# Performance work log

Hardware: AMD Instinct MI355X
Metric: run time of the kernel (lower is better)

Reference implementation:

```python
import jax, jax.numpy as jnp
import numpy as np

DIM = 384
HEADS = 12
HEAD_DIM = DIM // HEADS
WS = 7


def setup_inputs() -> dict:
    key = jax.random.key(0)
    k0, k1, k2, k3, k4 = jax.random.split(key, 5)
    x = jax.random.normal(k0, (16, DIM, 56, 56), dtype=jnp.float32)
    s = 1.0 / np.sqrt(DIM)
    Wqkv = jax.random.normal(k1, (DIM, 3 * DIM), dtype=jnp.float32) * s
    bqkv = jax.random.normal(k2, (3 * DIM,), dtype=jnp.float32) * 0.01
    Wproj = jax.random.normal(k3, (DIM, DIM), dtype=jnp.float32) * s
    bproj = jax.random.normal(k4, (DIM,), dtype=jnp.float32) * 0.01
    return {"x": x, "Wqkv": Wqkv, "bqkv": bqkv, "Wproj": Wproj, "bproj": bproj}


def _window_attention(x, Wqkv, bqkv, Wproj, bproj):
    B, D, H, W = x.shape
    x = jnp.transpose(x, (0, 2, 3, 1))  # (B, H, W, D)
    pad_h = (WS - H % WS) % WS
    pad_w = (WS - W % WS) % WS
    if pad_h or pad_w:
        x = jnp.pad(x, ((0, 0), (0, pad_h), (0, pad_w), (0, 0)))
    Hp, Wp = x.shape[1], x.shape[2]
    nH, nW = Hp // WS, Wp // WS
    # window partition: (B*nH*nW, WS*WS, D)
    xw = x.reshape(B, nH, WS, nW, WS, D).transpose(0, 1, 3, 2, 4, 5)
    windows = xw.reshape(B * nH * nW, WS * WS, D)
    BnW, N, _ = windows.shape
    qkv = windows @ Wqkv + bqkv  # (BnW, N, 3D)
    qkv = qkv.reshape(BnW, N, 3, HEADS, HEAD_DIM).transpose(2, 0, 3, 1, 4)
    q, k, v = qkv[0], qkv[1], qkv[2]  # (BnW, heads, N, hd)
    scale = HEAD_DIM ** -0.5
    attn = jnp.einsum('bhnd,bhmd->bhnm', q, k) * scale
    attn = jax.nn.softmax(attn, axis=-1)
    out = jnp.einsum('bhnm,bhmd->bhnd', attn, v)  # (BnW, heads, N, hd)
    out = out.transpose(0, 2, 1, 3).reshape(BnW, N, D)
    out = out @ Wproj + bproj
    # window reverse
    x = out.reshape(B, nH, nW, WS, WS, D).transpose(0, 1, 3, 2, 4, 5)
    x = x.reshape(B, Hp, Wp, D)
    if pad_h or pad_w:
        x = x[:, :H, :W, :]
    return jnp.transpose(x, (0, 3, 1, 2))  # (B, D, H, W)


def reference(x, Wqkv, bqkv, Wproj, bproj):
    return _window_attention(x, Wqkv, bqkv, Wproj, bproj)
```

## Files before the change

### kernel.cpp

```cpp
#include <hip/hip_runtime.h>

#define TOK     50176
#define NQKV    1152
#define DMODEL  384
#define HW      3136
#define NWIN    1024

typedef __bf16 bf16x8 __attribute__((ext_vector_type(8)));
typedef float  f32x4  __attribute__((ext_vector_type(4)));

__device__ __forceinline__ __bf16 f2bf(float f) {
  unsigned u = __float_as_uint(f);
  u += 0x7fffu + ((u >> 16) & 1u);
  unsigned short s = (unsigned short)(u >> 16);
  return __builtin_bit_cast(__bf16, s);
}
__device__ __forceinline__ unsigned short f2bfu(float f) {
  return __builtin_bit_cast(unsigned short, f2bf(f));
}
__device__ __forceinline__ float bf2f(__bf16 b) {
  return __uint_as_float(((unsigned)__builtin_bit_cast(unsigned short, b)) << 16);
}
__device__ __forceinline__ void gload_lds16(const void* g, void* l) {
  __builtin_amdgcn_global_load_lds(
      (const __attribute__((address_space(1))) unsigned int*)g,
      (__attribute__((address_space(3))) unsigned int*)l, 16, 0, 0);
}

__global__ __launch_bounds__(256) void gather_x(const float* __restrict__ x,
                                                __bf16* __restrict__ Xw) {
  __shared__ __bf16 lt[392 * 48];
  const int ct = blockIdx.x, hr = blockIdx.y, b = blockIdx.z;
  const int tid = threadIdx.x;
  const float* xb = x + ((size_t)(b * 384 + ct * 48)) * HW + hr * 7 * 56;

  for (int u = tid; u < 48 * 7 * 14; u += 256) {
    const int ch = u / 98, rem = u % 98;
    const int h7 = rem / 14, w4 = rem % 14;
    const float4 v = *(const float4*)&xb[(size_t)ch * HW + h7 * 56 + 4 * w4];
    const float vv[4] = {v.x, v.y, v.z, v.w};
#pragma unroll
    for (int e = 0; e < 4; ++e) {
      const int w = 4 * w4 + e;
      const int t = (w / 7) * 49 + h7 * 7 + (w % 7);
      lt[t * 48 + ch] = f2bf(vv[e]);
    }
  }
  __syncthreads();

  const size_t tokbase = (size_t)(b * 64 + hr * 8) * 49;
  for (int u = tid; u < 392 * 6; u += 256) {
    const int t = u / 6, c6 = u % 6;
    const bf16x8 vv = *(const bf16x8*)&lt[t * 48 + 8 * c6];
    *(bf16x8*)&Xw[(tokbase + t) * DMODEL + ct * 48 + 8 * c6] = vv;
  }
}

__global__ __launch_bounds__(256) void unscatter(const __bf16* __restrict__ P,
                                                 float* __restrict__ out) {
  __shared__ __bf16 lt[392 * 48];
  const int ct = blockIdx.x, hr = blockIdx.y, b = blockIdx.z;
  const int tid = threadIdx.x;
  const size_t tokbase = (size_t)(b * 64 + hr * 8) * 49;

  for (int u = tid; u < 392 * 6; u += 256) {
    const int t = u / 6, c6 = u % 6;
    *(bf16x8*)&lt[t * 48 + 8 * c6] =
        *(const bf16x8*)&P[(tokbase + t) * DMODEL + ct * 48 + 8 * c6];
  }
  __syncthreads();

  float* ob = out + ((size_t)(b * 384 + ct * 48)) * HW + hr * 7 * 56;
  for (int u = tid; u < 48 * 98; u += 256) {
    const int ch = u / 98, rem = u % 98;
    const int h7 = rem / 14, w4 = rem % 14;
    float4 o;
    float* oo = (float*)&o;
#pragma unroll
    for (int e = 0; e < 4; ++e) {
      const int w = 4 * w4 + e;
      const int t = (w / 7) * 49 + h7 * 7 + (w % 7);
      oo[e] = bf2f(lt[t * 48 + ch]);
    }
    *(float4*)&ob[(size_t)ch * HW + h7 * 56 + 4 * w4] = o;
  }
}

__global__ void conv_w(const float* __restrict__ Wqkv, const float* __restrict__ Wproj,
                       __bf16* __restrict__ WqkvT, __bf16* __restrict__ WprojT) {
  const int idx = blockIdx.x * 256 + threadIdx.x;
  if (idx < DMODEL * NQKV) {
    const int k = idx / NQKV, n = idx % NQKV;
    WqkvT[(size_t)n * DMODEL + k] = f2bf(Wqkv[idx]);
  }
  if (idx < DMODEL * DMODEL) {
    const int k = idx / DMODEL, n = idx % DMODEL;
    WprojT[(size_t)n * DMODEL + k] = f2bf(Wproj[idx]);
  }
}

__global__ __launch_bounds__(512) void gemm256(const __bf16* __restrict__ A,
                                               const __bf16* __restrict__ BT,
                                               const float* __restrict__ bias,
                                               __bf16* __restrict__ Cout, int Ncols) {
  __shared__ __align__(16) __bf16 As[2][256 * 32];
  __shared__ __align__(16) __bf16 Bs[2][128 * 32];
  const int tid  = threadIdx.x;
  const int lane = tid & 63;
  const int wid  = tid >> 6;

  const int nwg  = gridDim.x * gridDim.y;
  const int orig = blockIdx.y * gridDim.x + blockIdx.x;
  const int q    = nwg >> 3, r = nwg & 7;
  const int xcd  = orig & 7, pos = orig >> 3;
  const int start = (xcd < r) ? xcd * (q + 1) : r * (q + 1) + (xcd - r) * q;
  const int w    = start + pos;
  const int bn   = (w % gridDim.x) << 7;
  const int bm   = (w / gridDim.x) << 8;

  const __bf16* a0 = A  + (size_t)(bm +       (tid >> 2)) * DMODEL + ((tid & 3) << 3);
  const __bf16* a1 = A  + (size_t)(bm + 128 + (tid >> 2)) * DMODEL + ((tid & 3) << 3);
  const __bf16* b0 = BT + (size_t)(bn +       (tid >> 2)) * DMODEL + ((tid & 3) << 3);

  const int wm = (wid >> 1) << 6;
  const int wn = (wid & 1) << 6;
  const int lrow = lane & 15;
  const int lk8  = (lane >> 4) << 3;

  f32x4 acc[4][4] = {};

  auto stage = [&](int buf, int kt) {
    const int koff = kt << 5;
    gload_lds16(a0 + koff, &As[buf][(wid << 9)]);
    gload_lds16(a1 + koff, &As[buf][4096 + (wid << 9)]);
    gload_lds16(b0 + koff, &Bs[buf][(wid << 9)]);
  };

  stage(0, 0);
#pragma unroll 1
  for (int kt = 0; kt < 12; ++kt) {
    __syncthreads();
    if (kt + 1 < 12) stage((kt + 1) & 1, kt + 1);
    const __bf16* pA = &As[kt & 1][(wm + lrow) * 32 + lk8];
    const __bf16* pB = &Bs[kt & 1][(wn + lrow) * 32 + lk8];
    bf16x8 av[4], bv[4];
#pragma unroll
    for (int i = 0; i < 4; ++i) av[i] = *(const bf16x8*)(pA + i * 16 * 32);
#pragma unroll
    for (int j = 0; j < 4; ++j) bv[j] = *(const bf16x8*)(pB + j * 16 * 32);
#pragma unroll
    for (int i = 0; i < 4; ++i)
#pragma unroll
      for (int j = 0; j < 4; ++j)
        acc[j][i] = __builtin_amdgcn_mfma_f32_16x16x32_bf16(bv[j], av[i], acc[j][i], 0, 0, 0);
  }

  const int lr = lane & 15, g = lane >> 4;
  const int tok0 = bm + wm + lr;
  const int ch0  = bn + wn + (g << 2);

#pragma unroll
  for (int j = 0; j < 4; ++j) {
    const int ch = ch0 + 16 * j;
    const float4 b4 = *(const float4*)&bias[ch];
#pragma unroll
    for (int i = 0; i < 4; ++i) {
      const int token = tok0 + 16 * i;
      ushort4 pk;
      pk.x = f2bfu(acc[j][i][0] + b4.x);
      pk.y = f2bfu(acc[j][i][1] + b4.y);
      pk.z = f2bfu(acc[j][i][2] + b4.z);
      pk.w = f2bfu(acc[j][i][3] + b4.w);
      *(ushort4*)&Cout[(size_t)token * Ncols + ch] = pk;
    }
  }
}

__global__ __launch_bounds__(64) void attn_mfma(const __bf16* __restrict__ qkv,
                                                __bf16* __restrict__ attnO) {
  __shared__ __align__(16) __bf16 lds[96 * 72];
  __bf16* p_lds = lds;
  __bf16* vt    = lds + 64 * 72;

  const int lane = threadIdx.x;
  const int win  = blockIdx.x;
  const int h    = blockIdx.y;
  const int lr = lane & 15, g = lane >> 4;
  const size_t rowbase = (size_t)win * 49;

  int rr[4];
#pragma unroll
  for (int f = 0; f < 4; ++f) rr[f] = (16 * f + lr > 48) ? 48 : (16 * f + lr);

  const int co = h * 32 + 8 * g;

  bf16x8 av[4], bv[4];
#pragma unroll
  for (int f = 0; f < 4; ++f) {
    const __bf16* rp = qkv + (rowbase + rr[f]) * NQKV + co;
    av[f] = *(const bf16x8*)(rp + 384);
    bv[f] = *(const bf16x8*)(rp);
  }

  ushort4 vreg[7];
#pragma unroll
  for (int u = 0; u < 7; ++u) {
    const int unit = lane + (u << 6);
    if (unit < 392) {
      const int k = unit >> 3, dq = unit & 7;
      vreg[u] = *(const ushort4*)(qkv + (rowbase + k) * NQKV + 768 + h * 32 + 4 * dq);
    }
  }

  f32x4 acc[4][4] = {};
#pragma unroll
  for (int i = 0; i < 4; ++i)
#pragma unroll
    for (int j = 0; j < 4; ++j)
      acc[i][j] = __builtin_amdgcn_mfma_f32_16x16x32_bf16(av[i], bv[j], acc[i][j], 0, 0, 0);

  const float scale = 0.17677669529663687f;
#pragma unroll
  for (int i = 0; i < 4; ++i)
#pragma unroll
    for (int j = 0; j < 4; ++j)
#pragma unroll
      for (int r = 0; r < 4; ++r) {
        float v = acc[i][j][r] * scale;
        if (i == 3 && (4 * g + r) != 0) v = -1e30f;
        acc[i][j][r] = v;
      }

#pragma unroll
  for (int u = 0; u < 7; ++u) {
    const int unit = lane + (u << 6);
    if (unit < 392) {
      const int k = unit >> 3, dq = unit & 7;
      const ushort4 vv = vreg[u];
      vt[(4 * dq + 0) * 72 + k] = __builtin_bit_cast(__bf16, vv.x);
      vt[(4 * dq + 1) * 72 + k] = __builtin_bit_cast(__bf16, vv.y);
      vt[(4 * dq + 2) * 72 + k] = __builtin_bit_cast(__bf16, vv.z);
      vt[(4 * dq + 3) * 72 + k] = __builtin_bit_cast(__bf16, vv.w);
    }
  }

#pragma unroll
  for (int j = 0; j < 4; ++j) {
    float mx = -1e30f;
#pragma unroll
    for (int i = 0; i < 4; ++i)
#pragma unroll
      for (int r = 0; r < 4; ++r) mx = fmaxf(mx, acc[i][j][r]);
    mx = fmaxf(mx, __shfl_xor(mx, 16));
    mx = fmaxf(mx, __shfl_xor(mx, 32));
    float sum = 0.f;
#pragma unroll
    for (int i = 0; i < 4; ++i)
#pragma unroll
      for (int r = 0; r < 4; ++r) {
        const float e = __expf(acc[i][j][r] - mx);
        acc[i][j][r] = e;
        sum += e;
      }
    sum += __shfl_xor(sum, 16);
    sum += __shfl_xor(sum, 32);
    const float inv = 1.f / sum;
#pragma unroll
    for (int i = 0; i < 4; ++i) {
      ushort4 pk;
      pk.x = f2bfu(acc[i][j][0] * inv);
      pk.y = f2bfu(acc[i][j][1] * inv);
      pk.z = f2bfu(acc[i][j][2] * inv);
      pk.w = f2bfu(acc[i][j][3] * inv);
      *(ushort4*)&p_lds[(16 * j + lr) * 72 + 16 * i + 4 * g] = pk;
    }
  }

  f32x4 o[2][4] = {};
#pragma unroll
  for (int ks = 0; ks < 2; ++ks) {
    bf16x8 a2[2], b2[4];
#pragma unroll
    for (int i2 = 0; i2 < 2; ++i2)
      a2[i2] = *(const bf16x8*)&vt[(16 * i2 + lr) * 72 + 32 * ks + 8 * g];
#pragma unroll
    for (int j2 = 0; j2 < 4; ++j2)
      b2[j2] = *(const bf16x8*)&p_lds[(16 * j2 + lr) * 72 + 32 * ks + 8 * g];
#pragma unroll
    for (int i2 = 0; i2 < 2; ++i2)
#pragma unroll
      for (int j2 = 0; j2 < 4; ++j2)
        o[i2][j2] = __builtin_amdgcn_mfma_f32_16x16x32_bf16(a2[i2], b2[j2], o[i2][j2], 0, 0, 0);
  }

#pragma unroll
  for (int j2 = 0; j2 < 4; ++j2) {
    const int q = 16 * j2 + lr;
    if (q <= 48) {
#pragma unroll
      for (int i2 = 0; i2 < 2; ++i2) {
        ushort4 ok;
        ok.x = f2bfu(o[i2][j2][0]);
        ok.y = f2bfu(o[i2][j2][1]);
        ok.z = f2bfu(o[i2][j2][2]);
        ok.w = f2bfu(o[i2][j2][3]);
        *(ushort4*)&attnO[(rowbase + q) * DMODEL + h * 32 + 16 * i2 + 4 * g] = ok;
      }
    }
  }
}

extern "C" void kernel_launch(void* const* d_in, const int* in_sizes, int n_in,
                              void* d_out, int out_size, void* d_ws, size_t ws_size,
                              hipStream_t stream) {
  const float* x     = (const float*)d_in[0];
  const float* Wqkv  = (const float*)d_in[1];
  const float* bqkv  = (const float*)d_in[2];
  const float* Wproj = (const float*)d_in[3];
  const float* bproj = (const float*)d_in[4];
  float* out = (float*)d_out;

  char* ws = (char*)d_ws;
  __bf16* Xw     = (__bf16*)ws;  ws += (size_t)TOK * DMODEL * 2;
  __bf16* qkvb   = (__bf16*)ws;  ws += (size_t)TOK * NQKV * 2;
  __bf16* attnO  = (__bf16*)ws;  ws += (size_t)TOK * DMODEL * 2;
  __bf16* attnP  = (__bf16*)ws;  ws += (size_t)TOK * DMODEL * 2;
  __bf16* WqkvT  = (__bf16*)ws;  ws += (size_t)NQKV * DMODEL * 2;
  __bf16* WprojT = (__bf16*)ws;

  gather_x<<<dim3(8, 8, 16), 256, 0, stream>>>(x, Xw);
  conv_w<<<1728, 256, 0, stream>>>(Wqkv, Wproj, WqkvT, WprojT);
  gemm256<<<dim3(NQKV / 128, TOK / 256), 512, 0, stream>>>(Xw, WqkvT, bqkv, qkvb, NQKV);
  attn_mfma<<<dim3(NWIN, 12), 64, 0, stream>>>(qkvb, attnO);
  gemm256<<<dim3(DMODEL / 128, TOK / 256), 512, 0, stream>>>(attnO, WprojT, bproj, attnP, DMODEL);
  unscatter<<<dim3(8, 8, 16), 256, 0, stream>>>(attnP, out);
}
```

Measured before the change: 226.9 us.

## Replace LDS double-buffered GEMM with direct-global-load 128x128 tile GEMM

The GEMM kernel no longer stages A and B tiles through shared memory with double buffering and barriers. Each wave now loads its MFMA operands straight from global memory into registers, with the K loop fully unrolled, and the block tile shrinks from 256x128 to 128x128 with 256 threads. This removes LDS traffic and __syncthreads, but gives up cross-wave operand reuse. The result is heavier reliance on L1/L2 and possibly uncoalesced 16-byte row-strided loads.

```diff
diff --git a/kernel.cpp b/kernel.cpp
--- a/kernel.cpp
+++ b/kernel.cpp
@@ -20,11 +20,6 @@
 }
 __device__ __forceinline__ float bf2f(__bf16 b) {
   return __uint_as_float(((unsigned)__builtin_bit_cast(unsigned short, b)) << 16);
-}
-__device__ __forceinline__ void gload_lds16(const void* g, void* l) {
-  __builtin_amdgcn_global_load_lds(
-      (const __attribute__((address_space(1))) unsigned int*)g,
-      (__attribute__((address_space(3))) unsigned int*)l, 16, 0, 0);
 }
 
 __global__ __launch_bounds__(256) void gather_x(const float* __restrict__ x,
@@ -99,12 +94,10 @@
   }
 }
 
-__global__ __launch_bounds__(512) void gemm256(const __bf16* __restrict__ A,
-                                               const __bf16* __restrict__ BT,
-                                               const float* __restrict__ bias,
-                                               __bf16* __restrict__ Cout, int Ncols) {
-  __shared__ __align__(16) __bf16 As[2][256 * 32];
-  __shared__ __align__(16) __bf16 Bs[2][128 * 32];
+__global__ __launch_bounds__(256) void gemm_flat(const __bf16* __restrict__ A,
+                                                 const __bf16* __restrict__ BT,
+                                                 const float* __restrict__ bias,
+                                                 __bf16* __restrict__ Cout, int Ncols) {
   const int tid  = threadIdx.x;
   const int lane = tid & 63;
   const int wid  = tid >> 6;
@@ -116,38 +109,28 @@
   const int start = (xcd < r) ? xcd * (q + 1) : r * (q + 1) + (xcd - r) * q;
   const int w    = start + pos;
   const int bn   = (w % gridDim.x) << 7;
-  const int bm   = (w / gridDim.x) << 8;
-
-  const __bf16* a0 = A  + (size_t)(bm +       (tid >> 2)) * DMODEL + ((tid & 3) << 3);
-  const __bf16* a1 = A  + (size_t)(bm + 128 + (tid >> 2)) * DMODEL + ((tid & 3) << 3);
-  const __bf16* b0 = BT + (size_t)(bn +       (tid >> 2)) * DMODEL + ((tid & 3) << 3);
+  const int bm   = (w / gridDim.x) << 7;
 
   const int wm = (wid >> 1) << 6;
   const int wn = (wid & 1) << 6;
   const int lrow = lane & 15;
   const int lk8  = (lane >> 4) << 3;
 
+  const __bf16* pa = A  + (size_t)(bm + wm + lrow) * DMODEL + lk8;
+  const __bf16* pb = BT + (size_t)(bn + wn + lrow) * DMODEL + lk8;
+
   f32x4 acc[4][4] = {};
 
-  auto stage = [&](int buf, int kt) {
+#pragma unroll
+  for (int kt = 0; kt < 12; ++kt) {
     const int koff = kt << 5;
-    gload_lds16(a0 + koff, &As[buf][(wid << 9)]);
-    gload_lds16(a1 + koff, &As[buf][4096 + (wid << 9)]);
-    gload_lds16(b0 + koff, &Bs[buf][(wid << 9)]);
-  };
-
-  stage(0, 0);
-#pragma unroll 1
-  for (int kt = 0; kt < 12; ++kt) {
-    __syncthreads();
-    if (kt + 1 < 12) stage((kt + 1) & 1, kt + 1);
-    const __bf16* pA = &As[kt & 1][(wm + lrow) * 32 + lk8];
-    const __bf16* pB = &Bs[kt & 1][(wn + lrow) * 32 + lk8];
     bf16x8 av[4], bv[4];
 #pragma unroll
-    for (int i = 0; i < 4; ++i) av[i] = *(const bf16x8*)(pA + i * 16 * 32);
-#pragma unroll
-    for (int j = 0; j < 4; ++j) bv[j] = *(const bf16x8*)(pB + j * 16 * 32);
+    for (int i = 0; i < 4; ++i)
+      av[i] = *(const bf16x8*)(pa + (size_t)i * 16 * DMODEL + koff);
+#pragma unroll
+    for (int j = 0; j < 4; ++j)
+      bv[j] = *(const bf16x8*)(pb + (size_t)j * 16 * DMODEL + koff);
 #pragma unroll
     for (int i = 0; i < 4; ++i)
 #pragma unroll
@@ -330,8 +313,8 @@
 
   gather_x<<<dim3(8, 8, 16), 256, 0, stream>>>(x, Xw);
   conv_w<<<1728, 256, 0, stream>>>(Wqkv, Wproj, WqkvT, WprojT);
-  gemm256<<<dim3(NQKV / 128, TOK / 256), 512, 0, stream>>>(Xw, WqkvT, bqkv, qkvb, NQKV);
+  gemm_flat<<<dim3(NQKV / 128, TOK / 128), 256, 0, stream>>>(Xw, WqkvT, bqkv, qkvb, NQKV);
   attn_mfma<<<dim3(NWIN, 12), 64, 0, stream>>>(qkvb, attnO);
-  gemm256<<<dim3(DMODEL / 128, TOK / 256), 512, 0, stream>>>(attnO, WprojT, bproj, attnP, DMODEL);
+  gemm_flat<<<dim3(DMODEL / 128, TOK / 128), 256, 0, stream>>>(attnO, WprojT, bproj, attnP, DMODEL);
   unscatter<<<dim3(8, 8, 16), 256, 0, stream>>>(attnP, out);
 }
```

Result: slower. 337.8 us (+48.9%).
